# Kernel tuning notes

Measured on AMD Instinct MI355X. Metric: run time of the kernel, lower is better.

Reference implementation:

```python
import jax, jax.numpy as jnp
import numpy as np

N = 8192
D = 256  # hidden_size = in_features = out_features
NEG_SLOPE = 0.01  # nn.LeakyReLU() default
MASK_VAL = -1e12


def setup_inputs() -> dict:
    key = jax.random.key(0)
    k1, k2, k3, k4 = jax.random.split(key, 4)
    x = jax.random.normal(k1, (N, D), dtype=jnp.float32)
    adj = jax.random.randint(k2, (N, N), 0, 2, dtype=jnp.int32)
    # kaiming_uniform_ style params (scaled random uniform)
    W = jax.random.normal(k3, (D, D), dtype=jnp.float32) * (1.0 / np.sqrt(D))
    a = jax.random.normal(k4, (2 * D, 1), dtype=jnp.float32) * (1.0 / np.sqrt(2 * D))
    return {"x": x, "adj": adj, "W": W, "a": a}


def reference(x, adj, W, a):
    # GraphAttentionLayer.forward (eval mode: dropout is identity)
    h = x @ W  # [N, D]
    # a_input[i,j] = concat(h_i, h_j); a_input @ a decomposes as:
    #   e[i,j] = h_i . a[:D] + h_j . a[D:]
    # identical math without materializing the [N, N, 2D] tensor.
    e_src = h @ a[:D, 0]  # [N]
    e_dst = h @ a[D:, 0]  # [N]
    e = e_src[:, None] + e_dst[None, :]  # [N, N]
    e = jnp.where(e > 0, e, NEG_SLOPE * e)  # LeakyReLU
    att_logits = jnp.where(adj > 0, e, MASK_VAL)
    attention = jax.nn.softmax(att_logits, axis=1)
    h_prime = attention @ h  # [N, D]
    return jax.nn.elu(h_prime)  # concat=True branch
```

## Files before the change

### kernel.cpp

```cpp
#include <hip/hip_runtime.h>

#define NN 8192
#define DD 256

typedef __attribute__((ext_vector_type(8))) short short8;
typedef __attribute__((ext_vector_type(4))) float f32x4;

__device__ __forceinline__ short f2bf(float x) {
    union { float f; unsigned u; } v; v.f = x;
    unsigned r = (v.u + 0x7FFFu + ((v.u >> 16) & 1u)) >> 16;
    return (short)r;
}
__device__ __forceinline__ float bf2f(short b) {
    union { float f; unsigned u; } v; v.u = ((unsigned)(unsigned short)b) << 16;
    return v.f;
}

__global__ __launch_bounds__(256) void gat_prep(
    const float* __restrict__ x, const float* __restrict__ W,
    const float* __restrict__ a,
    short* __restrict__ hT, float* __restrict__ e_src, float* __restrict__ e_dst)
{
    __shared__ float x_s[32][260];
    __shared__ float W_s[2][16][256];
    const int t  = threadIdx.x;
    const int ib = blockIdx.x * 32;

    #pragma unroll
    for (int rep = 0; rep < 8; ++rep) {
        int fi = rep * 256 + t;
        int r  = fi >> 6;
        int c4 = (fi & 63) * 4;
        float4 v = *(const float4*)(x + (size_t)(ib + r) * DD + c4);
        *(float4*)&x_s[r][c4] = v;
    }
    float4 wp[4];
    #pragma unroll
    for (int q = 0; q < 4; ++q) {
        int fi = q * 256 + t;
        wp[q] = *(const float4*)(W + (size_t)(fi >> 6) * DD + (fi & 63) * 4);
    }
    __syncthreads();

    const int il = t >> 3;
    const int dg = (t & 7) * 4;
    f32x4 acc[8];
    #pragma unroll
    for (int m = 0; m < 8; ++m) acc[m] = (f32x4){0.f, 0.f, 0.f, 0.f};

    for (int kc = 0; kc < 16; ++kc) {
        const int b = kc & 1;
        #pragma unroll
        for (int q = 0; q < 4; ++q) {
            int fi = q * 256 + t;
            *(float4*)&W_s[b][fi >> 6][(fi & 63) * 4] = wp[q];
        }
        if (kc < 15) {
            #pragma unroll
            for (int q = 0; q < 4; ++q) {
                int fi = q * 256 + t;
                wp[q] = *(const float4*)(W + (size_t)((kc + 1) * 16 + (fi >> 6)) * DD + (fi & 63) * 4);
            }
        }
        __syncthreads();
        #pragma unroll
        for (int kl = 0; kl < 16; ++kl) {
            float xv = x_s[il][kc * 16 + kl];
            #pragma unroll
            for (int m = 0; m < 8; ++m) {
                float4 wv = *(const float4*)&W_s[b][kl][m * 32 + dg];
                acc[m].x += xv * wv.x; acc[m].y += xv * wv.y;
                acc[m].z += xv * wv.z; acc[m].w += xv * wv.w;
            }
        }
    }

    const int ig = ib + il;
    float p1 = 0.f, p2 = 0.f;
    #pragma unroll
    for (int m = 0; m < 8; ++m) {
        #pragma unroll
        for (int j = 0; j < 4; ++j) {
            int col = m * 32 + dg + j;
            float hv = acc[m][j];
            p1 += hv * a[col];
            p2 += hv * a[DD + col];
            hT[(size_t)col * NN + ig] = f2bf(hv);
        }
    }
    p1 += __shfl_xor(p1, 1); p1 += __shfl_xor(p1, 2); p1 += __shfl_xor(p1, 4);
    p2 += __shfl_xor(p2, 1); p2 += __shfl_xor(p2, 2); p2 += __shfl_xor(p2, 4);
    if ((t & 7) == 0) { e_src[ig] = p1; e_dst[ig] = p2; }
}

__global__ __launch_bounds__(512) void gat_main(
    const int* __restrict__ adj, const short* __restrict__ hT,
    const float* __restrict__ e_src, const float* __restrict__ e_dst,
    float* __restrict__ out)
{
    __shared__ __align__(16) short B_s[2][256][40];
    __shared__ __align__(16) short w_s[2][32][40];
    __shared__ float denom_s[32];

    const int t    = threadIdx.x;
    const int lane = t & 63;
    const int wid  = t >> 6;
    const int ibl  = blockIdx.x * 32;

    const int irow = t >> 4;
    const int jc2  = (t & 15) * 2;
    const float es = e_src[ibl + irow];
    const int* adj_row = adj + (size_t)(ibl + irow) * NN;
    const short* hrow = hT + (size_t)(t >> 1) * NN + (t & 1) * 16;

    const int ihalf = wid & 1;
    const int dbase = (wid >> 1) * 64;
    const int arow  = lane & 15;
    const int kg8   = (lane >> 4) * 8;

    float dsum = 0.f;
    f32x4 acc0 = {0.f,0.f,0.f,0.f}, acc1 = acc0, acc2 = acc0, acc3 = acc0;

    int2   adA = *(const int2*)(adj_row + jc2);
    float2 edA = *(const float2*)(e_dst + jc2);
    int4   h0A = *(const int4*)(hrow);
    int4   h1A = *(const int4*)(hrow + 8);
    int2   adB = *(const int2*)(adj_row + 32 + jc2);
    float2 edB = *(const float2*)(e_dst + 32 + jc2);
    int4   h0B = *(const int4*)(hrow + 32);
    int4   h1B = *(const int4*)(hrow + 32 + 8);

#define MAIN_STEP(AD, ED, H0, H1, n)                                           \
    {                                                                          \
        const int c = (n) & 1;                                                 \
        float s0 = es + ED.x, s1 = es + ED.y;                                  \
        float l0 = s0 > 0.f ? s0 : 0.01f * s0;                                 \
        float l1 = s1 > 0.f ? s1 : 0.01f * s1;                                 \
        float w0 = AD.x > 0 ? __expf(l0) : 0.f;                                \
        float w1 = AD.y > 0 ? __expf(l1) : 0.f;                                \
        short b0 = f2bf(w0), b1 = f2bf(w1);                                    \
        dsum += bf2f(b0) + bf2f(b1);    \
        *(unsigned*)&w_s[c][irow][jc2] =                                       \
            (unsigned)(unsigned short)b0 | ((unsigned)(unsigned short)b1 << 16);\
        *(int4*)&B_s[c][t >> 1][(t & 1) * 16]     = H0;                        \
        *(int4*)&B_s[c][t >> 1][(t & 1) * 16 + 8] = H1;                        \
        int jn = (((n) + 2) & (NN / 32 - 1)) * 32;       \
        AD = *(const int2*)(adj_row + jn + jc2);                               \
        ED = *(const float2*)(e_dst + jn + jc2);                               \
        H0 = *(const int4*)(hrow + jn);                                        \
        H1 = *(const int4*)(hrow + jn + 8);                                    \
        __syncthreads();                   \
        short8 af  = *(const short8*)&w_s[c][ihalf * 16 + arow][kg8];          \
        short8 bf0 = *(const short8*)&B_s[c][dbase +  0 + arow][kg8];          \
        short8 bf1 = *(const short8*)&B_s[c][dbase + 16 + arow][kg8];          \
        short8 bf2 = *(const short8*)&B_s[c][dbase + 32 + arow][kg8];          \
        short8 bf3 = *(const short8*)&B_s[c][dbase + 48 + arow][kg8];          \
        acc0 = __builtin_amdgcn_mfma_f32_16x16x32_bf16(af, bf0, acc0, 0, 0, 0);\
        acc1 = __builtin_amdgcn_mfma_f32_16x16x32_bf16(af, bf1, acc1, 0, 0, 0);\
        acc2 = __builtin_amdgcn_mfma_f32_16x16x32_bf16(af, bf2, acc2, 0, 0, 0);\
        acc3 = __builtin_amdgcn_mfma_f32_16x16x32_bf16(af, bf3, acc3, 0, 0, 0);\
    }

    for (int n = 0; n < NN / 32; n += 2) {
        MAIN_STEP(adA, edA, h0A, h1A, n)
        MAIN_STEP(adB, edB, h0B, h1B, n + 1)
    }
#undef MAIN_STEP

    dsum += __shfl_xor(dsum, 1);
    dsum += __shfl_xor(dsum, 2);
    dsum += __shfl_xor(dsum, 4);
    dsum += __shfl_xor(dsum, 8);
    if ((t & 15) == 0) denom_s[irow] = dsum;
    __syncthreads();

    const int rbase = ihalf * 16 + (lane >> 4) * 4;
    #pragma unroll
    for (int r = 0; r < 4; ++r) {
        float inv = 1.f / denom_s[rbase + r];
        size_t o = (size_t)(ibl + rbase + r) * DD + dbase + arow;
        float v0 = acc0[r] * inv; v0 = v0 > 0.f ? v0 : expm1f(v0);
        float v1 = acc1[r] * inv; v1 = v1 > 0.f ? v1 : expm1f(v1);
        float v2 = acc2[r] * inv; v2 = v2 > 0.f ? v2 : expm1f(v2);
        float v3 = acc3[r] * inv; v3 = v3 > 0.f ? v3 : expm1f(v3);
        out[o] = v0; out[o + 16] = v1; out[o + 32] = v2; out[o + 48] = v3;
    }
}

extern "C" void kernel_launch(void* const* d_in, const int* in_sizes, int n_in,
                              void* d_out, int out_size, void* d_ws, size_t ws_size,
                              hipStream_t stream) {
    const float* x   = (const float*)d_in[0];
    const int*   adj = (const int*)d_in[1];
    const float* W   = (const float*)d_in[2];
    const float* a   = (const float*)d_in[3];
    float* out = (float*)d_out;

    short* hT   = (short*)d_ws;
    float* esrc = (float*)((char*)d_ws + (size_t)DD * NN * 2);
    float* edst = esrc + NN;

    gat_prep<<<dim3(NN / 32), dim3(256), 0, stream>>>(x, W, a, hT, esrc, edst);
    gat_main<<<dim3(NN / 32), dim3(512), 0, stream>>>(adj, hT, esrc, edst, out);
}
```

Measured before the change: 209.9 us.

## Split attention key dimension across two blocks and combine in epilogue kernel

The main kernel now splits the neighbour (j) range in half, doubling the grid from 256 to 512 blocks so more CUs stay busy. Each half writes unnormalized numerators and partial denominators, and a new epilogue kernel sums them, normalizes, and applies ELU. Launch bounds also request 4 blocks per CU. The cost is an extra launch plus writing and re-reading two N×D float buffers. The softmax skips max subtraction, so the partial sums combine exactly.

```diff
diff --git a/kernel.cpp b/kernel.cpp
--- a/kernel.cpp
+++ b/kernel.cpp
@@ -2,6 +2,9 @@
 
 #define NN 8192
 #define DD 256
+#define JSPLIT 2
+#define JCH (NN / JSPLIT)
+#define NSTEP (JCH / 32)
 
 typedef __attribute__((ext_vector_type(8))) short short8;
 typedef __attribute__((ext_vector_type(4))) float f32x4;
@@ -93,25 +96,28 @@
     if ((t & 7) == 0) { e_src[ig] = p1; e_dst[ig] = p2; }
 }
 
-__global__ __launch_bounds__(512) void gat_main(
+__global__ __launch_bounds__(512, 4) void gat_main(
     const int* __restrict__ adj, const short* __restrict__ hT,
     const float* __restrict__ e_src, const float* __restrict__ e_dst,
-    float* __restrict__ out)
+    float* __restrict__ num0, float* __restrict__ num1,
+    float* __restrict__ den_part)
 {
     __shared__ __align__(16) short B_s[2][256][40];
     __shared__ __align__(16) short w_s[2][32][40];
-    __shared__ float denom_s[32];
 
     const int t    = threadIdx.x;
     const int lane = t & 63;
     const int wid  = t >> 6;
-    const int ibl  = blockIdx.x * 32;
+    const int ibl  = (blockIdx.x >> 1) * 32;
+    const int half = blockIdx.x & 1;
+    const int jb   = half * JCH;
 
     const int irow = t >> 4;
     const int jc2  = (t & 15) * 2;
     const float es = e_src[ibl + irow];
-    const int* adj_row = adj + (size_t)(ibl + irow) * NN;
-    const short* hrow = hT + (size_t)(t >> 1) * NN + (t & 1) * 16;
+    const int* adj_row = adj + (size_t)(ibl + irow) * NN + jb;
+    const short* hrow = hT + (size_t)(t >> 1) * NN + jb + (t & 1) * 16;
+    const float* edp = e_dst + jb;
 
     const int ihalf = wid & 1;
     const int dbase = (wid >> 1) * 64;
@@ -122,11 +128,11 @@
     f32x4 acc0 = {0.f,0.f,0.f,0.f}, acc1 = acc0, acc2 = acc0, acc3 = acc0;
 
     int2   adA = *(const int2*)(adj_row + jc2);
-    float2 edA = *(const float2*)(e_dst + jc2);
+    float2 edA = *(const float2*)(edp + jc2);
     int4   h0A = *(const int4*)(hrow);
     int4   h1A = *(const int4*)(hrow + 8);
     int2   adB = *(const int2*)(adj_row + 32 + jc2);
-    float2 edB = *(const float2*)(e_dst + 32 + jc2);
+    float2 edB = *(const float2*)(edp + 32 + jc2);
     int4   h0B = *(const int4*)(hrow + 32);
     int4   h1B = *(const int4*)(hrow + 32 + 8);
 
@@ -144,9 +150,9 @@
             (unsigned)(unsigned short)b0 | ((unsigned)(unsigned short)b1 << 16);\
         *(int4*)&B_s[c][t >> 1][(t & 1) * 16]     = H0;                        \
         *(int4*)&B_s[c][t >> 1][(t & 1) * 16 + 8] = H1;                        \
-        int jn = (((n) + 2) & (NN / 32 - 1)) * 32;       \
+        int jn = (((n) + 2) & (NSTEP - 1)) * 32;         \
         AD = *(const int2*)(adj_row + jn + jc2);                               \
-        ED = *(const float2*)(e_dst + jn + jc2);                               \
+        ED = *(const float2*)(edp + jn + jc2);                                 \
         H0 = *(const int4*)(hrow + jn);                                        \
         H1 = *(const int4*)(hrow + jn + 8);                                    \
         __syncthreads();                   \
@@ -161,7 +167,7 @@
         acc3 = __builtin_amdgcn_mfma_f32_16x16x32_bf16(af, bf3, acc3, 0, 0, 0);\
     }
 
-    for (int n = 0; n < NN / 32; n += 2) {
+    for (int n = 0; n < NSTEP; n += 2) {
         MAIN_STEP(adA, edA, h0A, h1A, n)
         MAIN_STEP(adB, edB, h0B, h1B, n + 1)
     }
@@ -171,20 +177,35 @@
     dsum += __shfl_xor(dsum, 2);
     dsum += __shfl_xor(dsum, 4);
     dsum += __shfl_xor(dsum, 8);
-    if ((t & 15) == 0) denom_s[irow] = dsum;
-    __syncthreads();
-
+    if ((t & 15) == 0) den_part[half * NN + ibl + irow] = dsum;
+
+    float* num = half ? num1 : num0;
     const int rbase = ihalf * 16 + (lane >> 4) * 4;
     #pragma unroll
     for (int r = 0; r < 4; ++r) {
-        float inv = 1.f / denom_s[rbase + r];
         size_t o = (size_t)(ibl + rbase + r) * DD + dbase + arow;
-        float v0 = acc0[r] * inv; v0 = v0 > 0.f ? v0 : expm1f(v0);
-        float v1 = acc1[r] * inv; v1 = v1 > 0.f ? v1 : expm1f(v1);
-        float v2 = acc2[r] * inv; v2 = v2 > 0.f ? v2 : expm1f(v2);
-        float v3 = acc3[r] * inv; v3 = v3 > 0.f ? v3 : expm1f(v3);
-        out[o] = v0; out[o + 16] = v1; out[o + 32] = v2; out[o + 48] = v3;
-    }
+        num[o]      = acc0[r];
+        num[o + 16] = acc1[r];
+        num[o + 32] = acc2[r];
+        num[o + 48] = acc3[r];
+    }
+}
+
+__global__ __launch_bounds__(256) void gat_epi(
+    float* __restrict__ out, const float* __restrict__ num1,
+    const float* __restrict__ den_part)
+{
+    int idx = blockIdx.x * 256 + threadIdx.x;
+    int row = idx >> 6;
+    float inv = 1.f / (den_part[row] + den_part[NN + row]);
+    float4 p0 = ((const float4*)out)[idx];
+    float4 p1 = ((const float4*)num1)[idx];
+    float4 v;
+    v.x = (p0.x + p1.x) * inv; v.x = v.x > 0.f ? v.x : expm1f(v.x);
+    v.y = (p0.y + p1.y) * inv; v.y = v.y > 0.f ? v.y : expm1f(v.y);
+    v.z = (p0.z + p1.z) * inv; v.z = v.z > 0.f ? v.z : expm1f(v.z);
+    v.w = (p0.w + p1.w) * inv; v.w = v.w > 0.f ? v.w : expm1f(v.w);
+    ((float4*)out)[idx] = v;
 }
 
 extern "C" void kernel_launch(void* const* d_in, const int* in_sizes, int n_in,
@@ -196,10 +217,15 @@
     const float* a   = (const float*)d_in[3];
     float* out = (float*)d_out;
 
-    short* hT   = (short*)d_ws;
-    float* esrc = (float*)((char*)d_ws + (size_t)DD * NN * 2);
+    char* w0 = (char*)d_ws;
+    short* hT   = (short*)w0;
+    float* esrc = (float*)(w0 + (size_t)DD * NN * 2);
     float* edst = esrc + NN;
+    float* den  = edst + NN;
+    float* num1 = den + 2 * NN;
 
     gat_prep<<<dim3(NN / 32), dim3(256), 0, stream>>>(x, W, a, hT, esrc, edst);
-    gat_main<<<dim3(NN / 32), dim3(512), 0, stream>>>(adj, hT, esrc, edst, out);
-}
+    gat_main<<<dim3((NN / 32) * JSPLIT), dim3(512), 0, stream>>>(
+        adj, hT, esrc, edst, out, num1, den);
+    gat_epi<<<dim3(NN * DD / 4 / 256), dim3(256), 0, stream>>>(out, num1, den);
+}
```

Result: slower. 217.1 us (+3.4%).
